# Kernel optimization log

Hardware: AMD Instinct MI355X
Metric: run time of the kernel (lower is better)

The kernel has to match this reference:

```python
import jax, jax.numpy as jnp
import numpy as np

B, S, D, H = 8, 1024, 768, 12
DH = D // H  # 64
EPS = 1e-12
NEG_INF = -1e30


def setup_inputs() -> dict:
    key = jax.random.key(0)
    ks = jax.random.split(key, 12)
    s = 0.02
    return {
        "hidden_states": jax.random.normal(ks[0], (B, S, D), jnp.float32),
        "attention_mask": jax.random.randint(ks[1], (B, 1, 1, S), 0, 2, jnp.int32),
        "Wq": jax.random.normal(ks[2], (D, D), jnp.float32) * s,
        "bq": jnp.zeros((D,), jnp.float32),
        "Wk": jax.random.normal(ks[3], (D, D), jnp.float32) * s,
        "bk": jnp.zeros((D,), jnp.float32),
        "Wv": jax.random.normal(ks[4], (D, D), jnp.float32) * s,
        "bv": jnp.zeros((D,), jnp.float32),
        "Wo": jax.random.normal(ks[5], (D, D), jnp.float32) * s,
        "bo": jnp.zeros((D,), jnp.float32),
        "ln_g": jnp.ones((D,), jnp.float32),
        "ln_b": jnp.zeros((D,), jnp.float32),
    }


def _split_heads(x):
    # [B,S,D] -> [B,H,S,DH]
    return x.reshape(B, S, H, DH).transpose(0, 2, 1, 3)


def reference(hidden_states, attention_mask, Wq, bq, Wk, bk, Wv, bv, Wo, bo, ln_g, ln_b):
    q = _split_heads(hidden_states @ Wq.T + bq)
    k = _split_heads(hidden_states @ Wk.T + bk)
    v = _split_heads(hidden_states @ Wv.T + bv)

    # scores: [B,H,S,S]
    scores = jnp.einsum("bhqd,bhkd->bhqk", q, k) / jnp.float32(np.sqrt(DH))
    mask0 = attention_mask == 0  # [B,1,1,S], broadcasts over heads/queries
    scores = jnp.where(mask0, NEG_INF, scores)
    probs = jax.nn.softmax(scores, axis=-1)
    # post-softmax masking (as in source)
    probs = jnp.where(mask0, 0.0, probs)

    ctx = jnp.einsum("bhqk,bhkd->bhqd", probs, v)
    ctx = ctx.transpose(0, 2, 1, 3).reshape(B, S, D)

    # BertSelfOutput: dense + residual + LayerNorm
    h = ctx @ Wo.T + bo + hidden_states
    mu = jnp.mean(h, axis=-1, keepdims=True)
    var = jnp.mean((h - mu) ** 2, axis=-1, keepdims=True)
    out = (h - mu) * jax.lax.rsqrt(var + EPS) * ln_g + ln_b
    return out, probs
```

## Files before the change

### kernel.cpp

```cpp
#include <hip/hip_runtime.h>

#define B_ 8
#define S_ 1024
#define D_ 768
#define H_ 12
#define DH_ 64

typedef __attribute__((ext_vector_type(8))) short short8;
typedef __attribute__((ext_vector_type(4))) short short4v;
typedef __attribute__((ext_vector_type(4))) float float4v;
typedef __attribute__((ext_vector_type(8))) __bf16 bf16x8;

static __device__ __forceinline__ short f2bf(float f) {
  union { float f; unsigned u; } v; v.f = f;
  unsigned r = v.u + 0x7fffu + ((v.u >> 16) & 1u);
  return (short)(r >> 16);
}
static __device__ __forceinline__ float bf2f(short s) {
  union { unsigned u; float f; } v; v.u = ((unsigned)(unsigned short)s) << 16;
  return v.f;
}

static __device__ __forceinline__ float4v mfma16(const short* ap, const short* bp, float4v c) {
  bf16x8 a = *(const bf16x8*)ap;
  bf16x8 b = *(const bf16x8*)bp;
  return __builtin_amdgcn_mfma_f32_16x16x32_bf16(a, b, c, 0, 0, 0);
}

typedef const __attribute__((address_space(1))) unsigned gu32;
typedef __attribute__((address_space(3))) unsigned lu32;
static __device__ __forceinline__ void gload16(const void* g, void* l) {
  __builtin_amdgcn_global_load_lds((gu32*)g, (lu32*)l, 16, 0, 0);
}

__global__ __launch_bounds__(256) void cvt_bf16(const float* __restrict__ src,
                                                short* __restrict__ dst, int n4) {
  int i = blockIdx.x * 256 + threadIdx.x;
  if (i < n4) {
    float4v v = ((const float4v*)src)[i];
    short4v o;
    o.x = f2bf(v.x); o.y = f2bf(v.y); o.z = f2bf(v.z); o.w = f2bf(v.w);
    ((short4v*)dst)[i] = o;
  }
}

__global__ __launch_bounds__(256) void gemm_qkv(const short* __restrict__ A,
                                                const short* __restrict__ Bw,
                                                const float* __restrict__ bq,
                                                const float* __restrict__ bk,
                                                const float* __restrict__ bv,
                                                short* __restrict__ Qb,
                                                short* __restrict__ Kb,
                                                short* __restrict__ Vtb) {
  __shared__ char smem[34816];
  short (*As)[32] = (short(*)[32])smem;
  short (*Bs)[32] = (short(*)[32])(smem + 8192);
  short (*Cs)[136] = (short(*)[136])smem;

  int m0 = blockIdx.x * 128, n0 = blockIdx.y * 128;
  int t = threadIdx.x, w = t >> 6, lane = t & 63;
  int wm = (w >> 1) * 64, wn = (w & 1) * 64;
  int lr = lane & 15, lk = (lane >> 4) * 8;

  const short* gA = A + (size_t)(m0 + w * 32 + (lane >> 2)) * 768 + (lane & 3) * 8;
  const short* gB = Bw + (size_t)(n0 + w * 32 + (lane >> 2)) * 768 + (lane & 3) * 8;

  float4v acc[4][4] = {};

  for (int k0 = 0; k0 < 768; k0 += 32) {
    gload16(gA, &As[w * 32][0]);
    gload16(gA + 16 * 768, &As[w * 32 + 16][0]);
    gload16(gB, &Bs[w * 32][0]);
    gload16(gB + 16 * 768, &Bs[w * 32 + 16][0]);
    gA += 32; gB += 32;
    __syncthreads();
    short8 a[4], b[4];
#pragma unroll
    for (int i = 0; i < 4; i++) a[i] = *(const short8*)&As[wm + i * 16 + lr][lk];
#pragma unroll
    for (int j = 0; j < 4; j++) b[j] = *(const short8*)&Bs[wn + j * 16 + lr][lk];
#pragma unroll
    for (int i = 0; i < 4; i++)
#pragma unroll
      for (int j = 0; j < 4; j++)
        acc[i][j] = mfma16((const short*)&a[i], (const short*)&b[j], acc[i][j]);
    __syncthreads();
  }

  int proj = blockIdx.y / 6;
  int nloc0 = n0 - proj * 768;
  int hhb = nloc0 >> 6;
  int b = m0 >> 10, s0v = m0 & 1023;

  if (proj < 2) {
    short* dst = (proj == 0) ? Qb : Kb;
    const float* bias = (proj == 0) ? bq : bk;
#pragma unroll
    for (int j = 0; j < 4; j++) {
      float bb = bias[nloc0 + wn + j * 16 + lr];
#pragma unroll
      for (int i = 0; i < 4; i++)
#pragma unroll
        for (int jj = 0; jj < 4; jj++)
          Cs[wm + i * 16 + (lane >> 4) * 4 + jj][wn + j * 16 + lr] = f2bf(acc[i][j][jj] + bb);
    }
    __syncthreads();
#pragma unroll
    for (int hh2 = 0; hh2 < 2; hh2++) {
      short* base = dst + ((size_t)(b * 12 + hhb + hh2) * 1024 + s0v) * 64;
#pragma unroll
      for (int u = 0; u < 4; u++) {
        int c = t + u * 256;
        int sl = c >> 3, dh0 = (c & 7) * 8;
        *(short8*)&base[(size_t)c * 8] = *(const short8*)&Cs[sl][hh2 * 64 + dh0];
      }
    }
  } else {
#pragma unroll
    for (int j = 0; j < 4; j++) {
      float bb = bv[nloc0 + wn + j * 16 + lr];
#pragma unroll
      for (int i = 0; i < 4; i++) {
        short4v p;
        p.x = f2bf(acc[i][j][0] + bb);
        p.y = f2bf(acc[i][j][1] + bb);
        p.z = f2bf(acc[i][j][2] + bb);
        p.w = f2bf(acc[i][j][3] + bb);
        *(short4v*)&Cs[wn + j * 16 + lr][wm + i * 16 + (lane >> 4) * 4] = p;
      }
    }
    __syncthreads();
#pragma unroll
    for (int u = 0; u < 8; u++) {
      int row = (t >> 4) + u * 16;
      int hh2 = row >> 6, dh = row & 63;
      *(short8*)&Vtb[((size_t)(b * 12 + hhb + hh2) * 64 + dh) * 1024 + s0v + (t & 15) * 8]
          = *(const short8*)&Cs[row][(t & 15) * 8];
    }
  }
}

__global__ __launch_bounds__(256) void attn_fused(const short* __restrict__ Qb,
                                                  const short* __restrict__ Kb,
                                                  const short* __restrict__ Vtb,
                                                  const int* __restrict__ amask,
                                                  float* __restrict__ probs,
                                                  short* __restrict__ ctxb) {
  __shared__ short P[16][1032];
  __shared__ float redmax[4][16];
  __shared__ float redsum[4][16];
  __shared__ float ctxp[4][16][64];

  int bh = blockIdx.y;
  int b = bh / 12, h = bh - b * 12;
  int q0 = blockIdx.x * 16;
  const short* Qp = Qb + ((size_t)bh * 1024 + q0) * 64;
  const short* Kp = Kb + (size_t)bh * 1024 * 64;
  const short* Vp = Vtb + (size_t)bh * 64 * 1024;
  const int* mb = amask + b * 1024;

  int t = threadIdx.x, w = t >> 6, lane = t & 63;
  int lr = lane & 15, lk = (lane >> 4) * 8;

  short8 aq0 = *(const short8*)&Qp[lr * 64 + lk];
  short8 aq1 = *(const short8*)&Qp[lr * 64 + 32 + lk];

  float4v acc[16] = {};
#pragma unroll
  for (int nt = 0; nt < 16; nt++) {
    const short* kp = Kp + (size_t)(w * 256 + nt * 16 + lr) * 64;
    short8 b0 = *(const short8*)&kp[lk];
    short8 b1 = *(const short8*)&kp[32 + lk];
    acc[nt] = mfma16((const short*)&aq0, (const short*)&b0, acc[nt]);
    acc[nt] = mfma16((const short*)&aq1, (const short*)&b1, acc[nt]);
  }

  unsigned mbits = 0;
#pragma unroll
  for (int nt = 0; nt < 16; nt++)
    mbits |= (mb[w * 256 + nt * 16 + lr] != 0 ? 1u : 0u) << nt;

  float mx[4] = {-1e30f, -1e30f, -1e30f, -1e30f};
#pragma unroll
  for (int nt = 0; nt < 16; nt++)
#pragma unroll
    for (int j = 0; j < 4; j++) {
      float s = acc[nt][j] * 0.125f;
      if (!((mbits >> nt) & 1)) s = -1e30f;
      acc[nt][j] = s;
      mx[j] = fmaxf(mx[j], s);
    }
#pragma unroll
  for (int j = 0; j < 4; j++) {
#pragma unroll
    for (int off = 1; off < 16; off <<= 1) mx[j] = fmaxf(mx[j], __shfl_xor(mx[j], off));
  }
  if (lr == 0) {
#pragma unroll
    for (int j = 0; j < 4; j++) redmax[w][(lane >> 4) * 4 + j] = mx[j];
  }
  __syncthreads();
  float gmx[4];
#pragma unroll
  for (int j = 0; j < 4; j++) {
    int r = (lane >> 4) * 4 + j;
    gmx[j] = fmaxf(fmaxf(redmax[0][r], redmax[1][r]), fmaxf(redmax[2][r], redmax[3][r]));
  }

  float sm[4] = {0.f, 0.f, 0.f, 0.f};
#pragma unroll
  for (int nt = 0; nt < 16; nt++)
#pragma unroll
    for (int j = 0; j < 4; j++) {
      float p = ((mbits >> nt) & 1) ? __expf(acc[nt][j] - gmx[j]) : 0.f;
      acc[nt][j] = p;
      sm[j] += p;
    }
#pragma unroll
  for (int j = 0; j < 4; j++) {
#pragma unroll
    for (int off = 1; off < 16; off <<= 1) sm[j] += __shfl_xor(sm[j], off);
  }
  if (lr == 0) {
#pragma unroll
    for (int j = 0; j < 4; j++) redsum[w][(lane >> 4) * 4 + j] = sm[j];
  }
  __syncthreads();
  float inv[4];
#pragma unroll
  for (int j = 0; j < 4; j++) {
    int r = (lane >> 4) * 4 + j;
    float s = redsum[0][r] + redsum[1][r] + redsum[2][r] + redsum[3][r];
    inv[j] = (s > 0.f) ? 1.f / s : 0.f;
  }

#pragma unroll
  for (int nt = 0; nt < 16; nt++) {
    int col = w * 256 + nt * 16 + lr;
#pragma unroll
    for (int j = 0; j < 4; j++) {
      int row = (lane >> 4) * 4 + j;
      P[row][col] = f2bf(acc[nt][j] * inv[j]);
    }
  }
  __syncthreads();

  size_t pbase = ((size_t)bh * 1024 + q0) * 1024;
  {
    int prow = t >> 4;
    int cb = (t & 15) * 4;
    float* orow = probs + pbase + (size_t)prow * 1024;
#pragma unroll
    for (int u = 0; u < 16; u++) {
      int col = cb + u * 64;
      short4v pv = *(const short4v*)&P[prow][col];
      float4v f;
      f.x = bf2f(pv.x); f.y = bf2f(pv.y); f.z = bf2f(pv.z); f.w = bf2f(pv.w);
      *(float4v*)&orow[col] = f;
    }
  }

  float4v c[4] = {};
#pragma unroll
  for (int ks = 0; ks < 8; ks++) {
    int kbase = w * 256 + ks * 32;
    short8 ap = *(const short8*)&P[lr][kbase + lk];
#pragma unroll
    for (int n2 = 0; n2 < 4; n2++) {
      short8 bvv = *(const short8*)&Vp[(size_t)(n2 * 16 + lr) * 1024 + kbase + lk];
      c[n2] = mfma16((const short*)&ap, (const short*)&bvv, c[n2]);
    }
  }
#pragma unroll
  for (int n2 = 0; n2 < 4; n2++)
#pragma unroll
    for (int j = 0; j < 4; j++)
      ctxp[w][(lane >> 4) * 4 + j][n2 * 16 + lr] = c[n2][j];
  __syncthreads();

  {
    int row = t >> 4, dh0 = (t & 15) * 4;
    short4v o4;
    float s0 = ctxp[0][row][dh0 + 0] + ctxp[1][row][dh0 + 0] + ctxp[2][row][dh0 + 0] + ctxp[3][row][dh0 + 0];
    float s1 = ctxp[0][row][dh0 + 1] + ctxp[1][row][dh0 + 1] + ctxp[2][row][dh0 + 1] + ctxp[3][row][dh0 + 1];
    float s2 = ctxp[0][row][dh0 + 2] + ctxp[1][row][dh0 + 2] + ctxp[2][row][dh0 + 2] + ctxp[3][row][dh0 + 2];
    float s3 = ctxp[0][row][dh0 + 3] + ctxp[1][row][dh0 + 3] + ctxp[2][row][dh0 + 3] + ctxp[3][row][dh0 + 3];
    o4.x = f2bf(s0); o4.y = f2bf(s1); o4.z = f2bf(s2); o4.w = f2bf(s3);
    *(short4v*)&ctxb[((size_t)(b * 1024 + q0 + row)) * 768 + h * 64 + dh0] = o4;
  }
}

__global__ __launch_bounds__(256) void gemm_o(const short* __restrict__ A,
                                              const short* __restrict__ Bw,
                                              const float* __restrict__ bo,
                                              const float* __restrict__ hidden,
                                              float* __restrict__ hout) {
  __shared__ short As[128][32];
  __shared__ short Bs[128][32];
  int m0 = blockIdx.x * 128, n0 = blockIdx.y * 128;
  int t = threadIdx.x, w = t >> 6, lane = t & 63;
  int wm = (w >> 1) * 64, wn = (w & 1) * 64;
  int lr = lane & 15, lk = (lane >> 4) * 8;

  const short* gA = A + (size_t)(m0 + w * 32 + (lane >> 2)) * 768 + (lane & 3) * 8;
  const short* gB = Bw + (size_t)(n0 + w * 32 + (lane >> 2)) * 768 + (lane & 3) * 8;

  float4v acc[4][4] = {};

  for (int k0 = 0; k0 < 768; k0 += 32) {
    gload16(gA, &As[w * 32][0]);
    gload16(gA + 16 * 768, &As[w * 32 + 16][0]);
    gload16(gB, &Bs[w * 32][0]);
    gload16(gB + 16 * 768, &Bs[w * 32 + 16][0]);
    gA += 32; gB += 32;
    __syncthreads();
    short8 a[4], b[4];
#pragma unroll
    for (int i = 0; i < 4; i++) a[i] = *(const short8*)&As[wm + i * 16 + lr][lk];
#pragma unroll
    for (int j = 0; j < 4; j++) b[j] = *(const short8*)&Bs[wn + j * 16 + lr][lk];
#pragma unroll
    for (int i = 0; i < 4; i++)
#pragma unroll
      for (int j = 0; j < 4; j++)
        acc[i][j] = mfma16((const short*)&a[i], (const short*)&b[j], acc[i][j]);
    __syncthreads();
  }

#pragma unroll
  for (int j = 0; j < 4; j++) {
    int gn = n0 + wn + j * 16 + lr;
    float bb = bo[gn];
#pragma unroll
    for (int i = 0; i < 4; i++) {
      int gm0 = m0 + wm + i * 16 + ((lane >> 4) << 2);
#pragma unroll
      for (int jj = 0; jj < 4; jj++) {
        int r = gm0 + jj;
        size_t idx = (size_t)r * 768 + gn;
        hout[idx] = acc[i][j][jj] + bb + hidden[idx];
      }
    }
  }
}

__global__ __launch_bounds__(256) void lnorm(const float* __restrict__ h,
                                             const float* __restrict__ g,
                                             const float* __restrict__ be,
                                             float* __restrict__ out) {
  int row = blockIdx.x;
  const float* x = h + (size_t)row * 768;
  int t = threadIdx.x;
  float v0 = x[t], v1 = x[t + 256], v2 = x[t + 512];
  float s = v0 + v1 + v2;
#pragma unroll
  for (int off = 1; off < 64; off <<= 1) s += __shfl_xor(s, off);
  __shared__ float r1[4], r2[4];
  if ((t & 63) == 0) r1[t >> 6] = s;
  __syncthreads();
  float mean = (r1[0] + r1[1] + r1[2] + r1[3]) * (1.f / 768.f);
  float d0 = v0 - mean, d1 = v1 - mean, d2 = v2 - mean;
  float q = d0 * d0 + d1 * d1 + d2 * d2;
#pragma unroll
  for (int off = 1; off < 64; off <<= 1) q += __shfl_xor(q, off);
  if ((t & 63) == 0) r2[t >> 6] = q;
  __syncthreads();
  float var = (r2[0] + r2[1] + r2[2] + r2[3]) * (1.f / 768.f);
  float rr = rsqrtf(var + 1e-12f);
  size_t o = (size_t)row * 768;
  out[o + t]       = d0 * rr * g[t] + be[t];
  out[o + t + 256] = d1 * rr * g[t + 256] + be[t + 256];
  out[o + t + 512] = d2 * rr * g[t + 512] + be[t + 512];
}

extern "C" void kernel_launch(void* const* d_in, const int* in_sizes, int n_in,
                              void* d_out, int out_size, void* d_ws, size_t ws_size,
                              hipStream_t stream) {
  const float* hs    = (const float*)d_in[0];
  const int*   amask = (const int*)d_in[1];
  const float* Wq    = (const float*)d_in[2];
  const float* bq    = (const float*)d_in[3];
  const float* Wk    = (const float*)d_in[4];
  const float* bk    = (const float*)d_in[5];
  const float* Wv    = (const float*)d_in[6];
  const float* bv    = (const float*)d_in[7];
  const float* Wo    = (const float*)d_in[8];
  const float* bo    = (const float*)d_in[9];
  const float* lng   = (const float*)d_in[10];
  const float* lnb   = (const float*)d_in[11];

  char* wsp = (char*)d_ws;
  const size_t NTOK = (size_t)B_ * S_;
  short* hsb  = (short*)wsp; wsp += NTOK * D_ * 2;
  short* wqkv = (short*)wsp; wsp += (size_t)3 * D_ * D_ * 2;
  short* wob  = (short*)wsp; wsp += (size_t)D_ * D_ * 2;
  short* Qb   = (short*)wsp; wsp += NTOK * D_ * 2;
  short* Kb   = (short*)wsp; wsp += NTOK * D_ * 2;
  short* Vtb  = (short*)wsp; wsp += NTOK * D_ * 2;
  short* ctxb = (short*)wsp; wsp += NTOK * D_ * 2;
  float* hbuf = (float*)wsp; wsp += NTOK * D_ * 4;

  float* out   = (float*)d_out;
  float* probs = out + NTOK * D_;

  int n4hs = (int)(NTOK * D_ / 4);
  cvt_bf16<<<dim3((n4hs + 255) / 256), dim3(256), 0, stream>>>(hs, hsb, n4hs);
  int n4w = D_ * D_ / 4;
  dim3 wg((n4w + 255) / 256);
  cvt_bf16<<<wg, dim3(256), 0, stream>>>(Wq, wqkv, n4w);
  cvt_bf16<<<wg, dim3(256), 0, stream>>>(Wk, wqkv + (size_t)D_ * D_, n4w);
  cvt_bf16<<<wg, dim3(256), 0, stream>>>(Wv, wqkv + (size_t)2 * D_ * D_, n4w);
  cvt_bf16<<<wg, dim3(256), 0, stream>>>(Wo, wob, n4w);

  gemm_qkv<<<dim3(64, 18), dim3(256), 0, stream>>>(hsb, wqkv, bq, bk, bv, Qb, Kb, Vtb);
  attn_fused<<<dim3(S_ / 16, B_ * H_), dim3(256), 0, stream>>>(Qb, Kb, Vtb, amask, probs, ctxb);
  gemm_o<<<dim3(64, 6), dim3(256), 0, stream>>>(ctxb, wob, bo, hs, hbuf);
  lnorm<<<dim3(8192), dim3(256), 0, stream>>>(hbuf, lng, lnb, out);
}
```

Baseline: 732.7 us.

## Restructure attention to per-wave full rows with three-pass QK recompute

Each wave now owns 16 query rows across the full key length, so the block-level shared-memory max and sum reductions and their barriers go away. QK^T is recomputed in three passes (max, sum, then normalized probabilities) instead of holding all scores in registers. Probabilities are staged in small per-wave chunks that feed both the fp32 probs store and the PV MFMA. The change also remaps workgroups for locality and merges the four weight-conversion launches into one, in exchange for roughly three times the QK MFMA work and K reads.

```diff
diff --git a/kernel.cpp b/kernel.cpp
--- a/kernel.cpp
+++ b/kernel.cpp
@@ -42,6 +42,22 @@
     o.x = f2bf(v.x); o.y = f2bf(v.y); o.z = f2bf(v.z); o.w = f2bf(v.w);
     ((short4v*)dst)[i] = o;
   }
+}
+
+__global__ __launch_bounds__(256) void cvt_w4(const float* __restrict__ w0,
+                                              const float* __restrict__ w1,
+                                              const float* __restrict__ w2,
+                                              const float* __restrict__ w3,
+                                              short* __restrict__ wqkv,
+                                              short* __restrict__ wob) {
+  int seg = blockIdx.x / 576, loc = blockIdx.x % 576;
+  const float* src = (seg == 0) ? w0 : (seg == 1) ? w1 : (seg == 2) ? w2 : w3;
+  short* dst = (seg < 3) ? (wqkv + (size_t)seg * 589824) : wob;
+  int i = loc * 256 + threadIdx.x;
+  float4v v = ((const float4v*)src)[i];
+  short4v o;
+  o.x = f2bf(v.x); o.y = f2bf(v.y); o.z = f2bf(v.z); o.w = f2bf(v.w);
+  ((short4v*)dst)[i] = o;
 }
 
 __global__ __launch_bounds__(256) void gemm_qkv(const short* __restrict__ A,
@@ -146,147 +162,126 @@
                                                   const int* __restrict__ amask,
                                                   float* __restrict__ probs,
                                                   short* __restrict__ ctxb) {
-  __shared__ short P[16][1032];
-  __shared__ float redmax[4][16];
-  __shared__ float redsum[4][16];
-  __shared__ float ctxp[4][16][64];
-
-  int bh = blockIdx.y;
+  __shared__ short Pw[4][16][136];
+
+  int orig = blockIdx.x;
+  int wg = (orig & 7) * 192 + (orig >> 3);
+  int bh = wg >> 4, qt = wg & 15;
   int b = bh / 12, h = bh - b * 12;
-  int q0 = blockIdx.x * 16;
+  int t = threadIdx.x, w = t >> 6, lane = t & 63;
+  int lr = lane & 15, lg = lane >> 4, lk = lg * 8;
+  int q0 = qt * 64 + w * 16;
+
   const short* Qp = Qb + ((size_t)bh * 1024 + q0) * 64;
-  const short* Kp = Kb + (size_t)bh * 1024 * 64;
-  const short* Vp = Vtb + (size_t)bh * 64 * 1024;
+  const short* Kp = Kb + (size_t)bh * 65536;
+  const short* Vp = Vtb + (size_t)bh * 65536;
   const int* mb = amask + b * 1024;
-
-  int t = threadIdx.x, w = t >> 6, lane = t & 63;
-  int lr = lane & 15, lk = (lane >> 4) * 8;
 
   short8 aq0 = *(const short8*)&Qp[lr * 64 + lk];
   short8 aq1 = *(const short8*)&Qp[lr * 64 + 32 + lk];
 
-  float4v acc[16] = {};
-#pragma unroll
-  for (int nt = 0; nt < 16; nt++) {
-    const short* kp = Kp + (size_t)(w * 256 + nt * 16 + lr) * 64;
+  unsigned long long mbits = 0ull;
+#pragma unroll 8
+  for (int nt = 0; nt < 64; nt++)
+    mbits |= (unsigned long long)(mb[nt * 16 + lr] != 0) << nt;
+
+  float mx[4] = {-1e30f, -1e30f, -1e30f, -1e30f};
+#pragma unroll 4
+  for (int nt = 0; nt < 64; nt++) {
+    const short* kp = Kp + (size_t)(nt * 16 + lr) * 64;
     short8 b0 = *(const short8*)&kp[lk];
     short8 b1 = *(const short8*)&kp[32 + lk];
-    acc[nt] = mfma16((const short*)&aq0, (const short*)&b0, acc[nt]);
-    acc[nt] = mfma16((const short*)&aq1, (const short*)&b1, acc[nt]);
-  }
-
-  unsigned mbits = 0;
-#pragma unroll
-  for (int nt = 0; nt < 16; nt++)
-    mbits |= (mb[w * 256 + nt * 16 + lr] != 0 ? 1u : 0u) << nt;
-
-  float mx[4] = {-1e30f, -1e30f, -1e30f, -1e30f};
-#pragma unroll
-  for (int nt = 0; nt < 16; nt++)
-#pragma unroll
-    for (int j = 0; j < 4; j++) {
-      float s = acc[nt][j] * 0.125f;
-      if (!((mbits >> nt) & 1)) s = -1e30f;
-      acc[nt][j] = s;
-      mx[j] = fmaxf(mx[j], s);
-    }
+    float4v s4 = {};
+    s4 = mfma16((const short*)&aq0, (const short*)&b0, s4);
+    s4 = mfma16((const short*)&aq1, (const short*)&b1, s4);
+    if ((mbits >> nt) & 1) {
+#pragma unroll
+      for (int j = 0; j < 4; j++) mx[j] = fmaxf(mx[j], s4[j] * 0.125f);
+    }
+  }
 #pragma unroll
   for (int j = 0; j < 4; j++) {
 #pragma unroll
     for (int off = 1; off < 16; off <<= 1) mx[j] = fmaxf(mx[j], __shfl_xor(mx[j], off));
   }
-  if (lr == 0) {
-#pragma unroll
-    for (int j = 0; j < 4; j++) redmax[w][(lane >> 4) * 4 + j] = mx[j];
-  }
-  __syncthreads();
-  float gmx[4];
+
+  float sm[4] = {0.f, 0.f, 0.f, 0.f};
+#pragma unroll 4
+  for (int nt = 0; nt < 64; nt++) {
+    const short* kp = Kp + (size_t)(nt * 16 + lr) * 64;
+    short8 b0 = *(const short8*)&kp[lk];
+    short8 b1 = *(const short8*)&kp[32 + lk];
+    float4v s4 = {};
+    s4 = mfma16((const short*)&aq0, (const short*)&b0, s4);
+    s4 = mfma16((const short*)&aq1, (const short*)&b1, s4);
+    if ((mbits >> nt) & 1) {
+#pragma unroll
+      for (int j = 0; j < 4; j++) sm[j] += __expf(s4[j] * 0.125f - mx[j]);
+    }
+  }
 #pragma unroll
   for (int j = 0; j < 4; j++) {
-    int r = (lane >> 4) * 4 + j;
-    gmx[j] = fmaxf(fmaxf(redmax[0][r], redmax[1][r]), fmaxf(redmax[2][r], redmax[3][r]));
-  }
-
-  float sm[4] = {0.f, 0.f, 0.f, 0.f};
-#pragma unroll
-  for (int nt = 0; nt < 16; nt++)
-#pragma unroll
-    for (int j = 0; j < 4; j++) {
-      float p = ((mbits >> nt) & 1) ? __expf(acc[nt][j] - gmx[j]) : 0.f;
-      acc[nt][j] = p;
-      sm[j] += p;
-    }
-#pragma unroll
-  for (int j = 0; j < 4; j++) {
 #pragma unroll
     for (int off = 1; off < 16; off <<= 1) sm[j] += __shfl_xor(sm[j], off);
   }
-  if (lr == 0) {
-#pragma unroll
-    for (int j = 0; j < 4; j++) redsum[w][(lane >> 4) * 4 + j] = sm[j];
-  }
-  __syncthreads();
   float inv[4];
 #pragma unroll
-  for (int j = 0; j < 4; j++) {
-    int r = (lane >> 4) * 4 + j;
-    float s = redsum[0][r] + redsum[1][r] + redsum[2][r] + redsum[3][r];
-    inv[j] = (s > 0.f) ? 1.f / s : 0.f;
-  }
-
-#pragma unroll
-  for (int nt = 0; nt < 16; nt++) {
-    int col = w * 256 + nt * 16 + lr;
-#pragma unroll
-    for (int j = 0; j < 4; j++) {
-      int row = (lane >> 4) * 4 + j;
-      P[row][col] = f2bf(acc[nt][j] * inv[j]);
-    }
-  }
-  __syncthreads();
-
+  for (int j = 0; j < 4; j++) inv[j] = (sm[j] > 0.f) ? 1.f / sm[j] : 0.f;
+
+  float4v c[4] = {};
   size_t pbase = ((size_t)bh * 1024 + q0) * 1024;
-  {
-    int prow = t >> 4;
-    int cb = (t & 15) * 4;
-    float* orow = probs + pbase + (size_t)prow * 1024;
-#pragma unroll
-    for (int u = 0; u < 16; u++) {
-      int col = cb + u * 64;
-      short4v pv = *(const short4v*)&P[prow][col];
+  for (int ch = 0; ch < 8; ch++) {
+#pragma unroll 2
+    for (int nt2 = 0; nt2 < 8; nt2++) {
+      int nt = ch * 8 + nt2;
+      const short* kp = Kp + (size_t)(nt * 16 + lr) * 64;
+      short8 b0 = *(const short8*)&kp[lk];
+      short8 b1 = *(const short8*)&kp[32 + lk];
+      float4v s4 = {};
+      s4 = mfma16((const short*)&aq0, (const short*)&b0, s4);
+      s4 = mfma16((const short*)&aq1, (const short*)&b1, s4);
+      bool live = (mbits >> nt) & 1;
+#pragma unroll
+      for (int j = 0; j < 4; j++) {
+        float p = live ? __expf(s4[j] * 0.125f - mx[j]) * inv[j] : 0.f;
+        Pw[w][lg * 4 + j][nt2 * 16 + lr] = f2bf(p);
+      }
+    }
+#pragma unroll
+    for (int u = 0; u < 8; u++) {
+      int slot = u * 64 + lane;
+      int r = slot >> 5, c4 = (slot & 31) * 4;
+      short4v pv = *(const short4v*)&Pw[w][r][c4];
       float4v f;
       f.x = bf2f(pv.x); f.y = bf2f(pv.y); f.z = bf2f(pv.z); f.w = bf2f(pv.w);
-      *(float4v*)&orow[col] = f;
-    }
-  }
-
-  float4v c[4] = {};
-#pragma unroll
-  for (int ks = 0; ks < 8; ks++) {
-    int kbase = w * 256 + ks * 32;
-    short8 ap = *(const short8*)&P[lr][kbase + lk];
-#pragma unroll
-    for (int n2 = 0; n2 < 4; n2++) {
-      short8 bvv = *(const short8*)&Vp[(size_t)(n2 * 16 + lr) * 1024 + kbase + lk];
-      c[n2] = mfma16((const short*)&ap, (const short*)&bvv, c[n2]);
-    }
-  }
+      *(float4v*)&probs[pbase + (size_t)r * 1024 + ch * 128 + c4] = f;
+    }
+#pragma unroll
+    for (int ks = 0; ks < 4; ks++) {
+      short8 ap = *(const short8*)&Pw[w][lr][ks * 32 + lk];
+#pragma unroll
+      for (int n2 = 0; n2 < 4; n2++) {
+        short8 bvv = *(const short8*)&Vp[(size_t)(n2 * 16 + lr) * 1024 + ch * 128 + ks * 32 + lk];
+        c[n2] = mfma16((const short*)&ap, (const short*)&bvv, c[n2]);
+      }
+    }
+  }
+
+  float (*cw)[68] = (float(*)[68])&Pw[w][0][0];
 #pragma unroll
   for (int n2 = 0; n2 < 4; n2++)
 #pragma unroll
     for (int j = 0; j < 4; j++)
-      ctxp[w][(lane >> 4) * 4 + j][n2 * 16 + lr] = c[n2][j];
-  __syncthreads();
-
-  {
-    int row = t >> 4, dh0 = (t & 15) * 4;
-    short4v o4;
-    float s0 = ctxp[0][row][dh0 + 0] + ctxp[1][row][dh0 + 0] + ctxp[2][row][dh0 + 0] + ctxp[3][row][dh0 + 0];
-    float s1 = ctxp[0][row][dh0 + 1] + ctxp[1][row][dh0 + 1] + ctxp[2][row][dh0 + 1] + ctxp[3][row][dh0 + 1];
-    float s2 = ctxp[0][row][dh0 + 2] + ctxp[1][row][dh0 + 2] + ctxp[2][row][dh0 + 2] + ctxp[3][row][dh0 + 2];
-    float s3 = ctxp[0][row][dh0 + 3] + ctxp[1][row][dh0 + 3] + ctxp[2][row][dh0 + 3] + ctxp[3][row][dh0 + 3];
-    o4.x = f2bf(s0); o4.y = f2bf(s1); o4.z = f2bf(s2); o4.w = f2bf(s3);
-    *(short4v*)&ctxb[((size_t)(b * 1024 + q0 + row)) * 768 + h * 64 + dh0] = o4;
+      cw[lg * 4 + j][n2 * 16 + lr] = c[n2][j];
+#pragma unroll
+  for (int u = 0; u < 2; u++) {
+    int idx = u * 64 + lane;
+    int r = idx >> 3, g = idx & 7;
+    const float* src = &cw[r][g * 8];
+    short8 o;
+    o[0] = f2bf(src[0]); o[1] = f2bf(src[1]); o[2] = f2bf(src[2]); o[3] = f2bf(src[3]);
+    o[4] = f2bf(src[4]); o[5] = f2bf(src[5]); o[6] = f2bf(src[6]); o[7] = f2bf(src[7]);
+    *(short8*)&ctxb[((size_t)(b * 1024 + q0 + r)) * 768 + h * 64 + g * 8] = o;
   }
 }
 
@@ -405,15 +400,10 @@
 
   int n4hs = (int)(NTOK * D_ / 4);
   cvt_bf16<<<dim3((n4hs + 255) / 256), dim3(256), 0, stream>>>(hs, hsb, n4hs);
-  int n4w = D_ * D_ / 4;
-  dim3 wg((n4w + 255) / 256);
-  cvt_bf16<<<wg, dim3(256), 0, stream>>>(Wq, wqkv, n4w);
-  cvt_bf16<<<wg, dim3(256), 0, stream>>>(Wk, wqkv + (size_t)D_ * D_, n4w);
-  cvt_bf16<<<wg, dim3(256), 0, stream>>>(Wv, wqkv + (size_t)2 * D_ * D_, n4w);
-  cvt_bf16<<<wg, dim3(256), 0, stream>>>(Wo, wob, n4w);
+  cvt_w4<<<dim3(4 * 576), dim3(256), 0, stream>>>(Wq, Wk, Wv, Wo, wqkv, wob);
 
   gemm_qkv<<<dim3(64, 18), dim3(256), 0, stream>>>(hsb, wqkv, bq, bk, bv, Qb, Kb, Vtb);
-  attn_fused<<<dim3(S_ / 16, B_ * H_), dim3(256), 0, stream>>>(Qb, Kb, Vtb, amask, probs, ctxb);
+  attn_fused<<<dim3(1536), dim3(256), 0, stream>>>(Qb, Kb, Vtb, amask, probs, ctxb);
   gemm_o<<<dim3(64, 6), dim3(256), 0, stream>>>(ctxb, wob, bo, hs, hbuf);
   lnorm<<<dim3(8192), dim3(256), 0, stream>>>(hbuf, lng, lnb, out);
 }
```

Measured after the change: 931.5 us. 27.1% more time.
